# Kernel tuning notes

Measured on AMD Instinct MI355X. Metric: run time of the kernel, lower is better.

## Reference

```python
import jax, jax.numpy as jnp
import numpy as np
from jax import lax

B, C, H, W = 256, 3, 224, 224
S = 20          # num_sample
M = 10          # mixture components
NFEAT = C + 2   # pixel channels + (x,y) loc
NHID = 100
NOUT = 10


def setup_inputs() -> dict:
    key = jax.random.key(0)
    ks = jax.random.split(key, 10)
    return {
        "x": jax.random.normal(ks[0], (B, C, H, W), jnp.float32),
        "u_cat": jax.random.uniform(ks[1], (S, B), jnp.float32),
        "z": jax.random.normal(ks[2], (S, B, 2), jnp.float32),
        "m_g_params": jax.random.normal(ks[3], (1, 6 * M), jnp.float32),
        "w_gc1": jax.random.uniform(ks[4], (NFEAT, NHID), jnp.float32, -0.1, 0.1),
        "b_gc1": jax.random.uniform(ks[5], (NHID,), jnp.float32, -0.1, 0.1),
        "w_gc2": jax.random.uniform(ks[6], (NHID, NOUT), jnp.float32, -0.3, 0.3),
        "b_gc2": jax.random.uniform(ks[7], (NOUT,), jnp.float32, -0.3, 0.3),
        "w_fcf": jax.random.uniform(ks[8], (NOUT * S, NOUT), jnp.float32, -0.07, 0.07),
        "b_fcf": jax.random.uniform(ks[9], (NOUT,), jnp.float32, -0.07, 0.07),
    }


def _forward(x, u_cat, z, m_g_params, w_gc1, b_gc1, w_gc2, b_gc2, w_fcf, b_fcf):
    # --- mixture params, replicating torch's split/stack/view reinterpretation ---
    pm = jnp.broadcast_to(m_g_params, (B, 6 * M)).reshape(B, M, 6).transpose(1, 0, 2)  # [M,B,6]
    pi = jax.nn.softmax(pm[:, :, 0].reshape(B, M), axis=-1)   # [B,M]
    mu_x = pm[:, :, 1].reshape(B, M)
    mu_y = pm[:, :, 2].reshape(B, M)
    lsig_x = pm[:, :, 3].reshape(B, M)
    lsig_y = pm[:, :, 4].reshape(B, M)
    rho = pm[:, :, 5].reshape(B, M)

    # --- categorical sampling via inverse CDF, vectorized over [S,B] ---
    cdf = jnp.cumsum(pi, axis=-1)                              # [B,M]
    idx = jnp.argmax(u_cat[:, :, None] < cdf[None, :, :], axis=-1)  # [S,B]
    bidx = jnp.arange(B)[None, :]                              # [1,B]
    mux = mu_x[bidx, idx]
    muy = mu_y[bidx, idx]
    sx = jnp.exp(lsig_x[bidx, idx])
    sy = jnp.exp(lsig_y[bidx, idx])
    r = jnp.tanh(rho[bidx, idx])

    # --- bivariate normal sample (Cholesky form); sample() is detached in torch ---
    z1, z2 = z[..., 0], z[..., 1]
    px = lax.stop_gradient(mux + sx * z1)
    py = lax.stop_gradient(muy + sy * (r * z1 + jnp.sqrt(1.0 - r * r) * z2))
    zx = (px - mux) / sx
    zy = (py - muy) / sy
    omr2 = 1.0 - r * r
    logprob = -(zx * zx - 2.0 * r * zx * zy + zy * zy) / (2.0 * omr2) \
              - jnp.log(2.0 * jnp.pi * sx * sy * jnp.sqrt(omr2))       # [S,B]
    loc = jnp.tanh(jnp.stack([px, py], axis=-1))               # [S,B,2]
    full_log_prob = jnp.sum(logprob, axis=0)                   # [B]

    # --- pixel gather (denormalize uses H for both coords, as in source) ---
    rows = jnp.clip(jnp.trunc(0.5 * (loc[..., 0] + 1.0) * H - 0.1).astype(jnp.int32), 0, H - 1)
    cols = jnp.clip(jnp.trunc(0.5 * (loc[..., 1] + 1.0) * H - 0.1).astype(jnp.int32), 0, W - 1)
    pix = x[bidx, :, rows, cols]                               # [S,B,C]

    samples = jnp.concatenate([pix, loc], axis=-1)             # [S,B,C+2]
    feat = samples.reshape(B, S, NFEAT)                        # torch .view reinterpretation

    # --- GCN with all-ones adjacency, eval mode (no dropout) ---
    adj = jnp.ones((S, S), feat.dtype)
    h = jax.nn.relu(jnp.matmul(adj, jnp.matmul(feat, w_gc1)) + b_gc1)  # [B,S,NHID]
    g = jnp.matmul(adj, jnp.matmul(h, w_gc2)) + b_gc2                  # [B,S,NOUT]
    g = jax.nn.log_softmax(g, axis=0)  # torch F.log_softmax default dim for 3D is 0

    logits = g.reshape(B, NOUT * S) @ w_fcf + b_fcf
    out = jax.nn.softmax(logits, axis=-1)                      # [B,NOUT]
    return out, full_log_prob


def reference(x, u_cat, z, m_g_params, w_gc1, b_gc1, w_gc2, b_gc2, w_fcf, b_fcf):
    return _forward(x, u_cat, z, m_g_params, w_gc1, b_gc1, w_gc2, b_gc2, w_fcf, b_fcf)
```

## Files before the change

### kernel.cpp

```cpp
#include <hip/hip_runtime.h>
#include <math.h>

#define Bn 256
#define Cn 3
#define Hn 224
#define Wn 224
#define Sn 20
#define Mn 10
#define NFEAT 5
#define NHID 100
#define NOUT 10
#define NT (Sn * Bn)

__global__ __launch_bounds__(64) void k_sample(
    const float* __restrict__ x, const float* __restrict__ u_cat,
    const float* __restrict__ z, const float* __restrict__ mg,
    float* __restrict__ samples, float* __restrict__ logprob)
{
    __shared__ float p[6 * Mn];
    __shared__ float bk[Mn][8];
    const int lt = threadIdx.x;
    const int t  = blockIdx.x * 64 + lt;
    const int bo = t & (Bn - 1);

    if (lt < 6 * Mn) p[lt] = mg[lt];
    __syncthreads();
    if (lt < Mn) {
        const float mux = p[lt * 6 + 1];
        const float muy = p[lt * 6 + 2];
        const float sx  = expf(p[lt * 6 + 3]);
        const float sy  = expf(p[lt * 6 + 4]);
        const float r   = tanhf(p[lt * 6 + 5]);
        const float sq  = sqrtf(1.f - r * r);
        bk[lt][0] = mux; bk[lt][1] = muy; bk[lt][2] = sx; bk[lt][3] = sy;
        bk[lt][4] = r;   bk[lt][5] = sq;
        bk[lt][6] = logf(6.283185307179586f * sx * sy * sq);
    }
    __syncthreads();

    float raw[Mn];
#pragma unroll
    for (int m = 0; m < Mn; ++m) raw[m] = p[((bo * Mn + m) >> 8) * 6 + 0];
    float mx = raw[0];
#pragma unroll
    for (int m = 1; m < Mn; ++m) mx = fmaxf(mx, raw[m]);
    float e[Mn];
    float sum = 0.f;
#pragma unroll
    for (int m = 0; m < Mn; ++m) { e[m] = expf(raw[m] - mx); sum += e[m]; }

    const float u = u_cat[t];
    float c = 0.f;
    int idx = 0;
    bool found = false;
#pragma unroll
    for (int m = 0; m < Mn; ++m) {
        c += e[m] / sum;
        if (!found && u < c) { idx = m; found = true; }
    }
    const int g = (bo * Mn + idx) >> 8;

    const float mux = bk[g][0], muy = bk[g][1];
    const float sx = bk[g][2], sy = bk[g][3];
    const float r = bk[g][4], sq = bk[g][5], lterm = bk[g][6];

    const float z1 = z[t * 2 + 0];
    const float z2 = z[t * 2 + 1];

    const float px = mux + sx * z1;
    const float py = muy + sy * (r * z1 + sq * z2);
    const float zx = (px - mux) / sx;
    const float zy = (py - muy) / sy;
    const float omr2 = 1.f - r * r;
    logprob[t] = -(zx * zx - 2.f * r * zx * zy + zy * zy) / (2.f * omr2) - lterm;

    const float lx = tanhf(px);
    const float ly = tanhf(py);
    const float vr = 0.5f * (lx + 1.f) * (float)Hn - 0.1f;
    const float vc = 0.5f * (ly + 1.f) * (float)Hn - 0.1f;
    int row = (int)vr; row = min(max(row, 0), Hn - 1);
    int col = (int)vc; col = min(max(col, 0), Wn - 1);

    const int base = bo * Cn * Hn * Wn + row * Wn + col;
    const int o5 = t * NFEAT;
    samples[o5 + 0] = x[base + 0 * Hn * Wn];
    samples[o5 + 1] = x[base + 1 * Hn * Wn];
    samples[o5 + 2] = x[base + 2 * Hn * Wn];
    samples[o5 + 3] = lx;
    samples[o5 + 4] = ly;
}

__global__ __launch_bounds__(256) void k_head(
    const float* __restrict__ samples, const float* __restrict__ logprob,
    const float* __restrict__ w1, const float* __restrict__ b1,
    const float* __restrict__ w2, const float* __restrict__ b2,
    const float* __restrict__ wf, const float* __restrict__ bf,
    float* __restrict__ out)
{
    const int b = threadIdx.x;
    __shared__ float sh_gv[NOUT][Bn];
    __shared__ float sh_part[NOUT][16];
    __shared__ float sh_max[NOUT];
    __shared__ float sh_lse[NOUT];
    __shared__ float sh_wsum[NOUT * NOUT];

    float flp = 0.f;
#pragma unroll
    for (int s = 0; s < Sn; ++s) flp += logprob[s * Bn + b];
    out[Bn * NOUT + b] = flp;

    float fs[NFEAT] = {0.f, 0.f, 0.f, 0.f, 0.f};
    const float4* sp4 = (const float4*)(samples + b * Sn * NFEAT);
#pragma unroll
    for (int v = 0; v < 25; ++v) {
        const float4 q = sp4[v];
        fs[(v * 4 + 0) % NFEAT] += q.x;
        fs[(v * 4 + 1) % NFEAT] += q.y;
        fs[(v * 4 + 2) % NFEAT] += q.z;
        fs[(v * 4 + 3) % NFEAT] += q.w;
    }

    float gv[NOUT];
#pragma unroll
    for (int k = 0; k < NOUT; ++k) gv[k] = 0.f;
    for (int j = 0; j < NHID; ++j) {
        float a = b1[j];
#pragma unroll
        for (int f = 0; f < NFEAT; ++f) a += fs[f] * w1[f * NHID + j];
        const float h = fmaxf(a, 0.f);
#pragma unroll
        for (int k = 0; k < NOUT; ++k) gv[k] += h * w2[j * NOUT + k];
    }
#pragma unroll
    for (int k = 0; k < NOUT; ++k) {
        gv[k] = (float)Sn * gv[k] + b2[k];
        sh_gv[k][b] = gv[k];
    }

    if (b < NOUT * NOUT) {
        const int k = b / NOUT, o = b % NOUT;
        float w = 0.f;
        for (int s = 0; s < Sn; ++s) w += wf[(s * NOUT + k) * NOUT + o];
        sh_wsum[b] = w;
    }
    __syncthreads();

    if (b < NOUT * 16) {
        const int k = b >> 4, part = b & 15;
        float m0 = sh_gv[k][part * 16];
        for (int i = 1; i < 16; ++i) m0 = fmaxf(m0, sh_gv[k][part * 16 + i]);
        sh_part[k][part] = m0;
    }
    __syncthreads();
    if (b < NOUT) {
        float m0 = sh_part[b][0];
        for (int i = 1; i < 16; ++i) m0 = fmaxf(m0, sh_part[b][i]);
        sh_max[b] = m0;
    }
    __syncthreads();
    if (b < NOUT * 16) {
        const int k = b >> 4, part = b & 15;
        const float m0 = sh_max[k];
        float sacc = 0.f;
        for (int i = 0; i < 16; ++i) sacc += expf(sh_gv[k][part * 16 + i] - m0);
        sh_part[k][part] = sacc;
    }
    __syncthreads();
    if (b < NOUT) {
        float sacc = 0.f;
        for (int i = 0; i < 16; ++i) sacc += sh_part[b][i];
        sh_lse[b] = sh_max[b] + logf(sacc);
    }
    __syncthreads();

    float lg[NOUT];
#pragma unroll
    for (int k = 0; k < NOUT; ++k) lg[k] = gv[k] - sh_lse[k];
    float logits[NOUT];
#pragma unroll
    for (int o = 0; o < NOUT; ++o) {
        float a = bf[o];
#pragma unroll
        for (int k = 0; k < NOUT; ++k) a += lg[k] * sh_wsum[k * NOUT + o];
        logits[o] = a;
    }
    float mxl = logits[0];
#pragma unroll
    for (int o = 1; o < NOUT; ++o) mxl = fmaxf(mxl, logits[o]);
    float ssum = 0.f;
#pragma unroll
    for (int o = 0; o < NOUT; ++o) { logits[o] = expf(logits[o] - mxl); ssum += logits[o]; }
#pragma unroll
    for (int o = 0; o < NOUT; ++o) out[b * NOUT + o] = logits[o] / ssum;
}

extern "C" void kernel_launch(void* const* d_in, const int* in_sizes, int n_in,
                              void* d_out, int out_size, void* d_ws, size_t ws_size,
                              hipStream_t stream) {
    const float* x   = (const float*)d_in[0];
    const float* u   = (const float*)d_in[1];
    const float* z   = (const float*)d_in[2];
    const float* mg  = (const float*)d_in[3];
    const float* w1  = (const float*)d_in[4];
    const float* b1  = (const float*)d_in[5];
    const float* w2  = (const float*)d_in[6];
    const float* b2  = (const float*)d_in[7];
    const float* wf  = (const float*)d_in[8];
    const float* bf  = (const float*)d_in[9];
    float* out = (float*)d_out;

    float* samples = (float*)d_ws;
    float* logprob = samples + NT * NFEAT;

    hipLaunchKernelGGL(k_sample, dim3(NT / 64), dim3(64), 0, stream,
                       x, u, z, mg, samples, logprob);
    hipLaunchKernelGGL(k_head, dim3(1), dim3(Bn), 0, stream,
                       samples, logprob, w1, b1, w2, b2, wf, bf, out);
}
```

Measured before the change: 235.0 us.

## Fuse sampling and head into one cooperative kernel with weight prefetch

Merges the sampling kernel and the single-block head kernel into one cooperative launch of 21 blocks. Twenty producer blocks each handle one sample index, while a consumer block stages the GCN weights into shared memory in a padded, vector-friendly layout and precomputes the wf sum. A grid-wide sync then lets the consumer run the head. This removes a kernel launch and hides the weight loads behind the sampling phase, at the cost of a cooperative launch and grid barrier overhead.

```diff
diff --git a/kernel.cpp b/kernel.cpp
--- a/kernel.cpp
+++ b/kernel.cpp
@@ -1,5 +1,8 @@
 #include <hip/hip_runtime.h>
+#include <hip/hip_cooperative_groups.h>
 #include <math.h>
+
+namespace cg = cooperative_groups;
 
 #define Bn 256
 #define Cn 3
@@ -10,99 +13,128 @@
 #define NFEAT 5
 #define NHID 100
 #define NOUT 10
-#define NT (Sn * Bn)
-
-__global__ __launch_bounds__(64) void k_sample(
+#define NPROD 20
+#define CONSUMER NPROD
+
+__global__ __launch_bounds__(256, 1) void k_all(
     const float* __restrict__ x, const float* __restrict__ u_cat,
     const float* __restrict__ z, const float* __restrict__ mg,
-    float* __restrict__ samples, float* __restrict__ logprob)
-{
-    __shared__ float p[6 * Mn];
-    __shared__ float bk[Mn][8];
-    const int lt = threadIdx.x;
-    const int t  = blockIdx.x * 64 + lt;
-    const int bo = t & (Bn - 1);
-
-    if (lt < 6 * Mn) p[lt] = mg[lt];
-    __syncthreads();
-    if (lt < Mn) {
-        const float mux = p[lt * 6 + 1];
-        const float muy = p[lt * 6 + 2];
-        const float sx  = expf(p[lt * 6 + 3]);
-        const float sy  = expf(p[lt * 6 + 4]);
-        const float r   = tanhf(p[lt * 6 + 5]);
-        const float sq  = sqrtf(1.f - r * r);
-        bk[lt][0] = mux; bk[lt][1] = muy; bk[lt][2] = sx; bk[lt][3] = sy;
-        bk[lt][4] = r;   bk[lt][5] = sq;
-        bk[lt][6] = logf(6.283185307179586f * sx * sy * sq);
-    }
-    __syncthreads();
-
-    float raw[Mn];
-#pragma unroll
-    for (int m = 0; m < Mn; ++m) raw[m] = p[((bo * Mn + m) >> 8) * 6 + 0];
-    float mx = raw[0];
-#pragma unroll
-    for (int m = 1; m < Mn; ++m) mx = fmaxf(mx, raw[m]);
-    float e[Mn];
-    float sum = 0.f;
-#pragma unroll
-    for (int m = 0; m < Mn; ++m) { e[m] = expf(raw[m] - mx); sum += e[m]; }
-
-    const float u = u_cat[t];
-    float c = 0.f;
-    int idx = 0;
-    bool found = false;
-#pragma unroll
-    for (int m = 0; m < Mn; ++m) {
-        c += e[m] / sum;
-        if (!found && u < c) { idx = m; found = true; }
-    }
-    const int g = (bo * Mn + idx) >> 8;
-
-    const float mux = bk[g][0], muy = bk[g][1];
-    const float sx = bk[g][2], sy = bk[g][3];
-    const float r = bk[g][4], sq = bk[g][5], lterm = bk[g][6];
-
-    const float z1 = z[t * 2 + 0];
-    const float z2 = z[t * 2 + 1];
-
-    const float px = mux + sx * z1;
-    const float py = muy + sy * (r * z1 + sq * z2);
-    const float zx = (px - mux) / sx;
-    const float zy = (py - muy) / sy;
-    const float omr2 = 1.f - r * r;
-    logprob[t] = -(zx * zx - 2.f * r * zx * zy + zy * zy) / (2.f * omr2) - lterm;
-
-    const float lx = tanhf(px);
-    const float ly = tanhf(py);
-    const float vr = 0.5f * (lx + 1.f) * (float)Hn - 0.1f;
-    const float vc = 0.5f * (ly + 1.f) * (float)Hn - 0.1f;
-    int row = (int)vr; row = min(max(row, 0), Hn - 1);
-    int col = (int)vc; col = min(max(col, 0), Wn - 1);
-
-    const int base = bo * Cn * Hn * Wn + row * Wn + col;
-    const int o5 = t * NFEAT;
-    samples[o5 + 0] = x[base + 0 * Hn * Wn];
-    samples[o5 + 1] = x[base + 1 * Hn * Wn];
-    samples[o5 + 2] = x[base + 2 * Hn * Wn];
-    samples[o5 + 3] = lx;
-    samples[o5 + 4] = ly;
-}
-
-__global__ __launch_bounds__(256) void k_head(
-    const float* __restrict__ samples, const float* __restrict__ logprob,
     const float* __restrict__ w1, const float* __restrict__ b1,
     const float* __restrict__ w2, const float* __restrict__ b2,
     const float* __restrict__ wf, const float* __restrict__ bf,
+    float* __restrict__ samples, float* __restrict__ logprob,
     float* __restrict__ out)
 {
-    const int b = threadIdx.x;
+    cg::grid_group grid = cg::this_grid();
+    const int blk = blockIdx.x;
+    const int tid = threadIdx.x;
+
+    __shared__ float p[6 * Mn];
+    __shared__ float bk[Mn][8];
+    __shared__ __align__(16) float b1L[NHID];
+    __shared__ __align__(16) float w1L[NHID * 8];
+    __shared__ __align__(16) float w2L[NHID * 16];
+    __shared__ float b2L[NOUT];
+    __shared__ float bfL[NOUT];
+    __shared__ float wsumL[NOUT * NOUT];
     __shared__ float sh_gv[NOUT][Bn];
     __shared__ float sh_part[NOUT][16];
     __shared__ float sh_max[NOUT];
     __shared__ float sh_lse[NOUT];
-    __shared__ float sh_wsum[NOUT * NOUT];
+
+    if (blk < NPROD) {
+        const int s = blk;
+        const int b = tid;
+        if (b < 6 * Mn) p[b] = mg[b];
+        __syncthreads();
+        if (b < Mn) {
+            const float mux = p[b * 6 + 1];
+            const float muy = p[b * 6 + 2];
+            const float sx  = expf(p[b * 6 + 3]);
+            const float sy  = expf(p[b * 6 + 4]);
+            const float r   = tanhf(p[b * 6 + 5]);
+            const float sq  = sqrtf(1.f - r * r);
+            bk[b][0] = mux; bk[b][1] = muy; bk[b][2] = sx; bk[b][3] = sy;
+            bk[b][4] = r;   bk[b][5] = sq;
+            bk[b][6] = logf(6.283185307179586f * sx * sy * sq);
+        }
+        __syncthreads();
+
+        float raw[Mn];
+#pragma unroll
+        for (int m = 0; m < Mn; ++m) raw[m] = p[((b * Mn + m) >> 8) * 6 + 0];
+        float mx = raw[0];
+#pragma unroll
+        for (int m = 1; m < Mn; ++m) mx = fmaxf(mx, raw[m]);
+        float e[Mn];
+        float sum = 0.f;
+#pragma unroll
+        for (int m = 0; m < Mn; ++m) { e[m] = expf(raw[m] - mx); sum += e[m]; }
+
+        const int t = s * Bn + b;
+        const float u = u_cat[t];
+        float c = 0.f;
+        int idx = 0;
+        bool found = false;
+#pragma unroll
+        for (int m = 0; m < Mn; ++m) {
+            c += e[m] / sum;
+            if (!found && u < c) { idx = m; found = true; }
+        }
+        const int g = (b * Mn + idx) >> 8;
+
+        const float mux = bk[g][0], muy = bk[g][1];
+        const float sx = bk[g][2], sy = bk[g][3];
+        const float r = bk[g][4], sq = bk[g][5], lterm = bk[g][6];
+
+        const float z1 = z[t * 2 + 0];
+        const float z2 = z[t * 2 + 1];
+
+        const float px = mux + sx * z1;
+        const float py = muy + sy * (r * z1 + sq * z2);
+        const float zx = (px - mux) / sx;
+        const float zy = (py - muy) / sy;
+        const float omr2 = 1.f - r * r;
+        logprob[t] = -(zx * zx - 2.f * r * zx * zy + zy * zy) / (2.f * omr2) - lterm;
+
+        const float lx = tanhf(px);
+        const float ly = tanhf(py);
+        const float vr = 0.5f * (lx + 1.f) * (float)Hn - 0.1f;
+        const float vc = 0.5f * (ly + 1.f) * (float)Hn - 0.1f;
+        int row = (int)vr; row = min(max(row, 0), Hn - 1);
+        int col = (int)vc; col = min(max(col, 0), Wn - 1);
+
+        const int base = b * Cn * Hn * Wn + row * Wn + col;
+        const int o5 = t * NFEAT;
+        samples[o5 + 0] = x[base + 0 * Hn * Wn];
+        samples[o5 + 1] = x[base + 1 * Hn * Wn];
+        samples[o5 + 2] = x[base + 2 * Hn * Wn];
+        samples[o5 + 3] = lx;
+        samples[o5 + 4] = ly;
+    } else {
+        for (int i = tid; i < NHID; i += 256) b1L[i] = b1[i];
+        for (int i = tid; i < NHID * NFEAT; i += 256) {
+            const int f = i / NHID, j = i % NHID;
+            w1L[j * 8 + f] = w1[i];
+        }
+        for (int i = tid; i < NHID * NOUT; i += 256) {
+            const int j = i / NOUT, k = i % NOUT;
+            w2L[j * 16 + k] = w2[i];
+        }
+        if (tid < NOUT) { b2L[tid] = b2[tid]; bfL[tid] = bf[tid]; }
+        if (tid < NOUT * NOUT) {
+            const int k = tid / NOUT, o = tid % NOUT;
+            float w = 0.f;
+            for (int s = 0; s < Sn; ++s) w += wf[(s * NOUT + k) * NOUT + o];
+            wsumL[tid] = w;
+        }
+    }
+
+    grid.sync();
+
+    if (blk != CONSUMER) return;
+
+    const int b = tid;
 
     float flp = 0.f;
 #pragma unroll
@@ -124,24 +156,22 @@
 #pragma unroll
     for (int k = 0; k < NOUT; ++k) gv[k] = 0.f;
     for (int j = 0; j < NHID; ++j) {
-        float a = b1[j];
-#pragma unroll
-        for (int f = 0; f < NFEAT; ++f) a += fs[f] * w1[f * NHID + j];
+        const float4 wa = *(const float4*)&w1L[j * 8];
+        const float  w4 = w1L[j * 8 + 4];
+        float a = b1L[j] + fs[0] * wa.x + fs[1] * wa.y + fs[2] * wa.z
+                         + fs[3] * wa.w + fs[4] * w4;
         const float h = fmaxf(a, 0.f);
-#pragma unroll
-        for (int k = 0; k < NOUT; ++k) gv[k] += h * w2[j * NOUT + k];
+        const float4 r0 = *(const float4*)&w2L[j * 16];
+        const float4 r1 = *(const float4*)&w2L[j * 16 + 4];
+        const float2 r2 = *(const float2*)&w2L[j * 16 + 8];
+        gv[0] += h * r0.x; gv[1] += h * r0.y; gv[2] += h * r0.z; gv[3] += h * r0.w;
+        gv[4] += h * r1.x; gv[5] += h * r1.y; gv[6] += h * r1.z; gv[7] += h * r1.w;
+        gv[8] += h * r2.x; gv[9] += h * r2.y;
     }
 #pragma unroll
     for (int k = 0; k < NOUT; ++k) {
-        gv[k] = (float)Sn * gv[k] + b2[k];
+        gv[k] = (float)Sn * gv[k] + b2L[k];
         sh_gv[k][b] = gv[k];
-    }
-
-    if (b < NOUT * NOUT) {
-        const int k = b / NOUT, o = b % NOUT;
-        float w = 0.f;
-        for (int s = 0; s < Sn; ++s) w += wf[(s * NOUT + k) * NOUT + o];
-        sh_wsum[b] = w;
     }
     __syncthreads();
 
@@ -179,9 +209,9 @@
     float logits[NOUT];
 #pragma unroll
     for (int o = 0; o < NOUT; ++o) {
-        float a = bf[o];
-#pragma unroll
-        for (int k = 0; k < NOUT; ++k) a += lg[k] * sh_wsum[k * NOUT + o];
+        float a = bfL[o];
+#pragma unroll
+        for (int k = 0; k < NOUT; ++k) a += lg[k] * wsumL[k * NOUT + o];
         logits[o] = a;
     }
     float mxl = logits[0];
@@ -210,10 +240,12 @@
     float* out = (float*)d_out;
 
     float* samples = (float*)d_ws;
-    float* logprob = samples + NT * NFEAT;
-
-    hipLaunchKernelGGL(k_sample, dim3(NT / 64), dim3(64), 0, stream,
-                       x, u, z, mg, samples, logprob);
-    hipLaunchKernelGGL(k_head, dim3(1), dim3(Bn), 0, stream,
-                       samples, logprob, w1, b1, w2, b2, wf, bf, out);
+    float* logprob = samples + Sn * Bn * NFEAT;
+
+    void* args[] = { (void*)&x, (void*)&u, (void*)&z, (void*)&mg,
+                     (void*)&w1, (void*)&b1, (void*)&w2, (void*)&b2,
+                     (void*)&wf, (void*)&bf,
+                     (void*)&samples, (void*)&logprob, (void*)&out };
+    hipLaunchCooperativeKernel((void*)k_all, dim3(NPROD + 1), dim3(Bn),
+                               args, 0, stream);
 }
```

New measurement: 241.1 us. 2.6% more time.
